# Performance work log

Hardware: AMD Instinct MI355X
Metric: run time of the kernel (lower is better)

The kernel has to match this reference:

```python
import jax, jax.numpy as jnp
import numpy as np

N_NODES = 50000
N_EDGES = 800000
D_NODE = 128
D_EDGE = 16
HID = 64
EPS = 1e-5


def _sage_conv(x, src, dst, Wl, bl, Wr, n_nodes):
    # PyG SAGEConv (mean aggr): out = lin_l(mean_{src->dst} x[src]) + lin_r(x)
    msg = x[src]                                        # [E, F] gather
    s = jax.ops.segment_sum(msg, dst, num_segments=n_nodes)   # [N, F]
    cnt = jax.ops.segment_sum(jnp.ones((src.shape[0],), x.dtype), dst,
                              num_segments=n_nodes)
    agg = s / jnp.maximum(cnt, 1.0)[:, None]
    return agg @ Wl.T + bl + x @ Wr.T


def _batchnorm(h, gamma, beta):
    # training-mode BN over node dim (biased variance, as in torch)
    mu = jnp.mean(h, axis=0)
    var = jnp.mean((h - mu) ** 2, axis=0)
    return gamma * (h - mu) / jnp.sqrt(var + EPS) + beta


def setup_inputs() -> dict:
    key = jax.random.key(0)
    ks = jax.random.split(key, 16)
    def lin(k, out_f, in_f):
        lim = 1.0 / np.sqrt(in_f)
        return jax.random.uniform(k, (out_f, in_f), jnp.float32, -lim, lim)
    x = jax.random.normal(ks[0], (N_NODES, D_NODE), jnp.float32)
    edge_index = jax.random.randint(ks[1], (2, N_EDGES), 0, N_NODES, jnp.int64)
    edge_attr = jax.random.normal(ks[2], (N_EDGES, D_EDGE), jnp.float32)
    return {
        "x": x, "edge_index": edge_index, "edge_attr": edge_attr,
        # SAGEConv 1
        "W1l": lin(ks[3], HID, D_NODE), "b1l": jnp.zeros((HID,), jnp.float32),
        "W1r": lin(ks[4], HID, D_NODE),
        "g1": jnp.ones((HID,), jnp.float32), "be1": jnp.zeros((HID,), jnp.float32),
        # SAGEConv 2
        "W2l": lin(ks[5], HID, HID), "b2l": jnp.zeros((HID,), jnp.float32),
        "W2r": lin(ks[6], HID, HID),
        "g2": jnp.ones((HID,), jnp.float32), "be2": jnp.zeros((HID,), jnp.float32),
        # edge MLP: (2*HID + D_EDGE) -> 128 -> 64 -> 2
        "Wm1": lin(ks[7], 128, 2 * HID + D_EDGE), "bm1": jnp.zeros((128,), jnp.float32),
        "Wm2": lin(ks[8], 64, 128), "bm2": jnp.zeros((64,), jnp.float32),
        "Wm3": lin(ks[9], 2, 64), "bm3": jnp.zeros((2,), jnp.float32),
    }


def reference(x, edge_index, edge_attr,
              W1l, b1l, W1r, g1, be1,
              W2l, b2l, W2r, g2, be2,
              Wm1, bm1, Wm2, bm2, Wm3, bm3):
    src, dst = edge_index[0], edge_index[1]
    n = x.shape[0]
    h = _sage_conv(x, src, dst, W1l, b1l, W1r, n)
    h = jax.nn.relu(_batchnorm(h, g1, be1))          # dropout = identity (eval)
    h = _sage_conv(h, src, dst, W2l, b2l, W2r, n)
    h = jax.nn.relu(_batchnorm(h, g2, be2))
    edge_in = jnp.concatenate([h[src], edge_attr, h[dst]], axis=1)  # [E, 144]
    z = jax.nn.relu(edge_in @ Wm1.T + bm1)
    z = jax.nn.relu(z @ Wm2.T + bm2)
    return z @ Wm3.T + bm3                           # [E, 2] logits
```

## Files before the change

kernel.cpp:

```cpp
#include <hip/hip_runtime.h>
#include <hip/hip_fp16.h>


#define EPS 1e-5f

typedef _Float16 h8 __attribute__((ext_vector_type(8)));
typedef float f32x4 __attribute__((ext_vector_type(4)));

__global__ __launch_bounds__(256) void k_prep_hist(
    const float* __restrict__ W1l, const float* __restrict__ W1r,
    const float* __restrict__ b1l,
    const float* __restrict__ W2l, const float* __restrict__ W2r,
    const float* __restrict__ b2l,
    const float* __restrict__ Wm1, const float* __restrict__ Wm2,
    float* __restrict__ Wt1, float* __restrict__ Wt2,
    float* __restrict__ bias1, float* __restrict__ bias2,
    __half* __restrict__ W2B, __half* __restrict__ W1B,
    const int* __restrict__ dst, int* __restrict__ deg, int E, int prepBlocks) {
  if ((int)blockIdx.x >= prepBlocks) {
    int e = (blockIdx.x - prepBlocks) * 256 + threadIdx.x;
    if (e < E) atomicAdd(&deg[dst[e]], 1);
    return;
  }
  int idx = blockIdx.x * 256 + threadIdx.x;
  if (idx < 16384) {
    int k = idx >> 7, f = idx & 127;
    Wt1[idx] = (f < 64) ? W1l[f * 128 + k] : W1r[(f - 64) * 128 + k];
    return;
  }
  idx -= 16384;
  if (idx < 8192) {
    int k = idx >> 7, f = idx & 127;
    Wt2[idx] = (f < 64) ? W2l[f * 64 + k] : W2r[(f - 64) * 64 + k];
    return;
  }
  idx -= 8192;
  if (idx < 128) { bias1[idx] = (idx < 64) ? 0.f : b1l[idx - 64]; return; }
  idx -= 128;
  if (idx < 128) { bias2[idx] = (idx < 64) ? 0.f : b2l[idx - 64]; return; }
  idx -= 128;
  if (idx < 8192) {
    int j = idx & 7, l = (idx >> 3) & 63, f = idx >> 9;
    int kc = f >> 2, tt = f & 3;
    int col = 16 * tt + (l & 15);
    int k = 32 * kc + (l >> 4) * 8 + j;
    W2B[idx] = __float2half(Wm2[col * 128 + k]);
    return;
  }
  idx -= 8192;
  if (idx < 20480) {
    int j = idx & 7, l = (idx >> 3) & 63, f = idx >> 9;
    int kc = f >> 3, nc = f & 7;
    int k = 32 * kc + (l >> 4) * 8 + j;
    int n = 16 * nc + (l & 15);
    float w;
    if (k < 64)       w = Wm1[n * 144 + k];
    else if (k < 128) w = Wm1[n * 144 + 80 + (k - 64)];
    else if (k < 144) w = Wm1[n * 144 + 64 + (k - 128)];
    else              w = 0.f;
    W1B[idx] = __float2half(w);
    return;
  }
}

__global__ __launch_bounds__(1024) void k_scan(
    const int* __restrict__ deg, int* __restrict__ rowptr,
    int* __restrict__ cursor, int N) {
  __shared__ int wsum[16];
  __shared__ int carry;
  const int lane = threadIdx.x & 63;
  const int w    = threadIdx.x >> 6;
  if (threadIdx.x == 0) carry = 0;
  __syncthreads();
  for (int base = 0; base < N; base += 1024) {
    int i = base + threadIdx.x;
    int v = (i < N) ? deg[i] : 0;
    int incl = v;
#pragma unroll
    for (int off = 1; off < 64; off <<= 1) {
      int t = __shfl_up(incl, off);
      if (lane >= off) incl += t;
    }
    if (lane == 63) wsum[w] = incl;
    __syncthreads();
    if (w == 0) {
      int ws_ = (lane < 16) ? wsum[lane] : 0;
      int wincl = ws_;
#pragma unroll
      for (int off = 1; off < 16; off <<= 1) {
        int t = __shfl_up(wincl, off);
        if (lane >= off) wincl += t;
      }
      if (lane < 16) wsum[lane] = wincl;
    }
    __syncthreads();
    int woff = carry + (w > 0 ? wsum[w - 1] : 0);
    int excl = woff + incl - v;
    if (i < N) { rowptr[i] = excl; cursor[i] = excl; }
    int tot = wsum[15];
    __syncthreads();
    if (threadIdx.x == 0) carry += tot;
    __syncthreads();
  }
  if (threadIdx.x == 0) rowptr[N] = carry;
}

__global__ __launch_bounds__(256) void k_fill(
    const int* __restrict__ src, const int* __restrict__ dst,
    const float* __restrict__ attr,
    int* __restrict__ cursor, int* __restrict__ csr_src,
    int* __restrict__ csr_dst, int* __restrict__ pos,
    __half* __restrict__ attrC, int E) {
  int e = blockIdx.x * 256 + threadIdx.x;
  if (e < E) {
    int d = dst[e];
    int p = atomicAdd(&cursor[d], 1);
    csr_src[p] = src[e];
    csr_dst[p] = d;
    pos[e] = p;
    const float4* at4 = (const float4*)attr;
    float4 a0 = at4[(size_t)e * 4 + 0];
    float4 a1 = at4[(size_t)e * 4 + 1];
    float4 a2 = at4[(size_t)e * 4 + 2];
    float4 a3 = at4[(size_t)e * 4 + 3];
    __half2 hh[8];
    hh[0] = __floats2half2_rn(a0.x, a0.y);
    hh[1] = __floats2half2_rn(a0.z, a0.w);
    hh[2] = __floats2half2_rn(a1.x, a1.y);
    hh[3] = __floats2half2_rn(a1.z, a1.w);
    hh[4] = __floats2half2_rn(a2.x, a2.y);
    hh[5] = __floats2half2_rn(a2.z, a2.w);
    hh[6] = __floats2half2_rn(a3.x, a3.y);
    hh[7] = __floats2half2_rn(a3.z, a3.w);
    *(uint4*)&attrC[(size_t)p * 16]     = *(uint4*)&hh[0];
    *(uint4*)&attrC[(size_t)p * 16 + 8] = *(uint4*)&hh[4];
  }
}

__global__ __launch_bounds__(256) void k_scatter_out(
    const float* __restrict__ out2, const int* __restrict__ pos,
    float* __restrict__ out, int E) {
  int e = blockIdx.x * 256 + threadIdx.x;
  if (e < E) {
    int p = pos[e];
    *(float2*)&out[(size_t)e * 2] = *(const float2*)&out2[(size_t)p * 2];
  }
}

template<int K, int MODE>
__global__ __launch_bounds__(256) void k_gemm(
    const float* __restrict__ X, const float* __restrict__ stats,
    const float* __restrict__ Wt, const float* __restrict__ bias,
    __half* __restrict__ outH, float* __restrict__ outF, int N, int Ftot) {
  __shared__ __align__(16) float Xs[32][68];
  __shared__ __align__(16) float Ws_[32][128];
  const int tid = threadIdx.x;
  const int tx  = tid & 15;
  const int ty  = tid >> 4;
  const int n0  = blockIdx.x * 64;
  float acc[4][8];
#pragma unroll
  for (int j = 0; j < 8; ++j) {
    float bv = bias[8 * tx + j];
#pragma unroll
    for (int i = 0; i < 4; ++i) acc[i][j] = bv;
  }
  for (int k0 = 0; k0 < K; k0 += 32) {
    __syncthreads();
#pragma unroll
    for (int l = 0; l < 2; ++l) {
      int idx = tid * 2 + l;
      int kq = idx & 7, n = idx >> 3;
      float4 xv = make_float4(0.f, 0.f, 0.f, 0.f);
      if (n0 + n < N) xv = *(const float4*)&X[(size_t)(n0 + n) * K + k0 + kq * 4];
      if (stats) {
        int kb = k0 + kq * 4;
        xv.x = fmaxf(xv.x * stats[128 + kb + 0] + stats[192 + kb + 0], 0.f);
        xv.y = fmaxf(xv.y * stats[128 + kb + 1] + stats[192 + kb + 1], 0.f);
        xv.z = fmaxf(xv.z * stats[128 + kb + 2] + stats[192 + kb + 2], 0.f);
        xv.w = fmaxf(xv.w * stats[128 + kb + 3] + stats[192 + kb + 3], 0.f);
      }
      Xs[kq * 4 + 0][n] = xv.x;
      Xs[kq * 4 + 1][n] = xv.y;
      Xs[kq * 4 + 2][n] = xv.z;
      Xs[kq * 4 + 3][n] = xv.w;
    }
#pragma unroll
    for (int l = 0; l < 4; ++l) {
      int idx = tid + l * 256;
      int kr = idx >> 5, fc = idx & 31;
      *(float4*)&Ws_[kr][fc * 4] =
          *(const float4*)&Wt[(size_t)(k0 + kr) * Ftot + fc * 4];
    }
    __syncthreads();
#pragma unroll
    for (int kk = 0; kk < 32; ++kk) {
      float4 a  = *(const float4*)&Xs[kk][4 * ty];
      float4 b0 = *(const float4*)&Ws_[kk][8 * tx];
      float4 b1 = *(const float4*)&Ws_[kk][8 * tx + 4];
      float aa[4] = {a.x, a.y, a.z, a.w};
      float bb[8] = {b0.x, b0.y, b0.z, b0.w, b1.x, b1.y, b1.z, b1.w};
#pragma unroll
      for (int i = 0; i < 4; ++i)
#pragma unroll
        for (int j = 0; j < 8; ++j) acc[i][j] += aa[i] * bb[j];
    }
  }
#pragma unroll
  for (int i = 0; i < 4; ++i) {
    int n = n0 + 4 * ty + i;
    if (n >= N) continue;
    if (tx < 8) {
      __half2 hh[4];
#pragma unroll
      for (int c = 0; c < 4; ++c)
        hh[c] = __floats2half2_rn(acc[i][2 * c], acc[i][2 * c + 1]);
      *(uint4*)&outH[(size_t)n * 64 + 8 * tx] = *(uint4*)hh;
    } else {
      float* cp = outF + (size_t)n * 64 + 8 * tx - 64;
      *(float4*)cp = make_float4(acc[i][0], acc[i][1], acc[i][2], acc[i][3]);
      *(float4*)(cp + 4) = make_float4(acc[i][4], acc[i][5], acc[i][6], acc[i][7]);
    }
  }
}

__global__ __launch_bounds__(256) void k_agg(
    const __half* __restrict__ qb, const float* __restrict__ pb,
    const int* __restrict__ rowptr, const int* __restrict__ csr_src,
    float* __restrict__ hpre, float* __restrict__ stats, int N) {
  __shared__ float red[512];
  const int tid  = threadIdx.x;
  const int w    = tid >> 6;
  const int lane = tid & 63;
  const int g    = lane >> 3, c = lane & 7;
  float lsum = 0.f, lsq = 0.f;
  const int wid = blockIdx.x * 4 + w;
  const int nw  = gridDim.x * 4;
  for (int n = wid; n < N; n += nw) {
    const int r0 = rowptr[n], r1 = rowptr[n + 1];
    float s[8] = {0.f, 0.f, 0.f, 0.f, 0.f, 0.f, 0.f, 0.f};
    for (int j = r0 + g; j < r1; j += 8) {
      int a = csr_src[j];
      uint4 rv = *(const uint4*)&qb[(size_t)a * 64 + 8 * c];
      const __half2* hp = (const __half2*)&rv;
#pragma unroll
      for (int q = 0; q < 4; ++q) {
        float2 f2 = __half22float2(hp[q]);
        s[2 * q]     += f2.x;
        s[2 * q + 1] += f2.y;
      }
    }
#pragma unroll
    for (int m = 8; m < 64; m <<= 1)
#pragma unroll
      for (int q = 0; q < 8; ++q) s[q] += __shfl_xor(s[q], m);
    float sv = s[0];
#pragma unroll
    for (int q = 1; q < 8; ++q) sv = (g == q) ? s[q] : sv;
    float cdeg = (float)(r1 - r0);
    cdeg = cdeg > 1.f ? cdeg : 1.f;
    const int f = 8 * c + g;
    float v = sv / cdeg + pb[(size_t)n * 64 + f];
    hpre[(size_t)n * 64 + f] = v;
    lsum += v;
    lsq  += v * v;
  }
  red[tid]       = lsum;
  red[256 + tid] = lsq;
  __syncthreads();
  if (tid < 64) {
    float ts = red[tid] + red[tid + 64] + red[tid + 128] + red[tid + 192];
    float tq = red[256 + tid] + red[256 + tid + 64] + red[256 + tid + 128] + red[256 + tid + 192];
    int f = 8 * (tid & 7) + (tid >> 3);
    atomicAdd(&stats[f], ts);
    atomicAdd(&stats[64 + f], tq);
  }
}

__global__ void k_finalize(float* stats, const float* __restrict__ g,
                           const float* __restrict__ be, int N) {
  int f = threadIdx.x;
  float inv_n = 1.0f / (float)N;
  float mean = stats[f] * inv_n;
  float var  = stats[64 + f] * inv_n - mean * mean;
  float s = g[f] * rsqrtf(var + EPS);
  stats[128 + f] = s;
  stats[192 + f] = be[f] - mean * s;
}

__global__ __launch_bounds__(256) void k_bn(
    const float* __restrict__ H1, const float* __restrict__ stats,
    __half* __restrict__ H2, int N) {
  int idx = blockIdx.x * 256 + threadIdx.x;
  if (idx >= N * 8) return;
  int n = idx >> 3, f8 = (idx & 7) * 8;
  float4 h0 = *(const float4*)&H1[(size_t)n * 64 + f8];
  float4 h1 = *(const float4*)&H1[(size_t)n * 64 + f8 + 4];
  const float* sc = stats + 128 + f8;
  const float* sh = stats + 192 + f8;
  __half2 hh[4];
  hh[0] = __floats2half2_rn(fmaxf(h0.x * sc[0] + sh[0], 0.f),
                            fmaxf(h0.y * sc[1] + sh[1], 0.f));
  hh[1] = __floats2half2_rn(fmaxf(h0.z * sc[2] + sh[2], 0.f),
                            fmaxf(h0.w * sc[3] + sh[3], 0.f));
  hh[2] = __floats2half2_rn(fmaxf(h1.x * sc[4] + sh[4], 0.f),
                            fmaxf(h1.y * sc[5] + sh[5], 0.f));
  hh[3] = __floats2half2_rn(fmaxf(h1.z * sc[6] + sh[6], 0.f),
                            fmaxf(h1.w * sc[7] + sh[7], 0.f));
  *(uint4*)&H2[(size_t)n * 64 + f8] = *(uint4*)hh;
}

__global__ __launch_bounds__(256, 2) void k_edge(
    const __half* __restrict__ H2, const __half* __restrict__ attrC,
    const int* __restrict__ csrc, const int* __restrict__ cdst,
    const __half* __restrict__ W1Bws, const __half* __restrict__ W2Bws,
    const float* __restrict__ bm1, const float* __restrict__ bm2,
    const float* __restrict__ Wm3, const float* __restrict__ bm3,
    float* __restrict__ out2, int E) {
  __shared__ __align__(16) _Float16 W1B[20480];
  __shared__ __align__(16) _Float16 W2B[8192];
  __shared__ __align__(16) _Float16 Z1f[64 * 136];

  const int tid  = threadIdx.x;
  const int lane = tid & 63;
  const int w    = tid >> 6;
  const int ln15 = lane & 15;
  const int quad = lane >> 4;

  for (int i = tid; i < 2560; i += 256)
    ((uint4*)W1B)[i] = ((const uint4*)W1Bws)[i];
  for (int i = tid; i < 1024; i += 256)
    ((uint4*)W2B)[i] = ((const uint4*)W2Bws)[i];

  float bm1v[8];
#pragma unroll
  for (int nc = 0; nc < 8; ++nc) bm1v[nc] = bm1[16 * nc + ln15];
  float bmv[4], w30[4], w31[4];
#pragma unroll
  for (int t = 0; t < 4; ++t) {
    bmv[t] = bm2[16 * t + ln15];
    w30[t] = Wm3[16 * t + ln15];
    w31[t] = Wm3[64 + 16 * t + ln15];
  }
  const float bm30 = bm3[0], bm31 = bm3[1];
  __syncthreads();

  const int nt = (E + 63) >> 6;
  const int rowoff = 16 * w + ln15;

  for (int t = blockIdx.x; t < nt; t += gridDim.x) {
    int er = (t << 6) + rowoff;
    if (er >= E) er = E - 1;
    const int s = csrc[er];
    const int d = cdst[er];

    h8 af0 = *(const h8*)&H2[(size_t)s * 64 + 8 * quad];
    h8 af1 = *(const h8*)&H2[(size_t)s * 64 + 32 + 8 * quad];
    h8 af2 = *(const h8*)&H2[(size_t)d * 64 + 8 * quad];
    h8 af3 = *(const h8*)&H2[(size_t)d * 64 + 32 + 8 * quad];
    h8 af4 = (h8){0, 0, 0, 0, 0, 0, 0, 0};
    if (quad < 2)
      af4 = *(const h8*)&attrC[(size_t)er * 16 + 8 * quad];

    f32x4 acc1[8];
#pragma unroll
    for (int nc = 0; nc < 8; ++nc)
      acc1[nc] = (f32x4){bm1v[nc], bm1v[nc], bm1v[nc], bm1v[nc]};
#pragma unroll
    for (int nc = 0; nc < 8; ++nc)
      acc1[nc] = __builtin_amdgcn_mfma_f32_16x16x32_f16(
          af0, *(const h8*)&W1B[((0 * 8 + nc) << 9) + (lane << 3)], acc1[nc], 0, 0, 0);
#pragma unroll
    for (int nc = 0; nc < 8; ++nc)
      acc1[nc] = __builtin_amdgcn_mfma_f32_16x16x32_f16(
          af1, *(const h8*)&W1B[((1 * 8 + nc) << 9) + (lane << 3)], acc1[nc], 0, 0, 0);
#pragma unroll
    for (int nc = 0; nc < 8; ++nc)
      acc1[nc] = __builtin_amdgcn_mfma_f32_16x16x32_f16(
          af2, *(const h8*)&W1B[((2 * 8 + nc) << 9) + (lane << 3)], acc1[nc], 0, 0, 0);
#pragma unroll
    for (int nc = 0; nc < 8; ++nc)
      acc1[nc] = __builtin_amdgcn_mfma_f32_16x16x32_f16(
          af3, *(const h8*)&W1B[((3 * 8 + nc) << 9) + (lane << 3)], acc1[nc], 0, 0, 0);
#pragma unroll
    for (int nc = 0; nc < 8; ++nc)
      acc1[nc] = __builtin_amdgcn_mfma_f32_16x16x32_f16(
          af4, *(const h8*)&W1B[((4 * 8 + nc) << 9) + (lane << 3)], acc1[nc], 0, 0, 0);

    const int ebase = 16 * w + 4 * quad;
#pragma unroll
    for (int nc = 0; nc < 8; ++nc)
#pragma unroll
      for (int r = 0; r < 4; ++r)
        Z1f[(ebase + r) * 136 + 16 * nc + ln15] =
            (_Float16)fmaxf(acc1[nc][r], 0.f);

    f32x4 acc2[4];
#pragma unroll
    for (int tt = 0; tt < 4; ++tt)
      acc2[tt] = (f32x4){bmv[tt], bmv[tt], bmv[tt], bmv[tt]};
#pragma unroll
    for (int kc = 0; kc < 4; ++kc) {
      h8 a = *(const h8*)&Z1f[(16 * w + ln15) * 136 + 32 * kc + 8 * quad];
#pragma unroll
      for (int tt = 0; tt < 4; ++tt) {
        h8 bf = *(const h8*)&W2B[((kc * 4 + tt) * 64 + lane) * 8];
        acc2[tt] = __builtin_amdgcn_mfma_f32_16x16x32_f16(a, bf, acc2[tt], 0, 0, 0);
      }
    }

    float p0[4], p1[4];
#pragma unroll
    for (int r = 0; r < 4; ++r) { p0[r] = 0.f; p1[r] = 0.f; }
#pragma unroll
    for (int tt = 0; tt < 4; ++tt)
#pragma unroll
      for (int r = 0; r < 4; ++r) {
        float z = fmaxf(acc2[tt][r], 0.f);
        p0[r] += z * w30[tt];
        p1[r] += z * w31[tt];
      }
#pragma unroll
    for (int r = 0; r < 4; ++r) {
#pragma unroll
      for (int m = 1; m < 16; m <<= 1) {
        p0[r] += __shfl_xor(p0[r], m);
        p1[r] += __shfl_xor(p1[r], m);
      }
      if (ln15 == 0) {
        int j = (t << 6) + 16 * w + 4 * quad + r;
        if (j < E)
          *(float2*)&out2[(size_t)j * 2] = make_float2(p0[r] + bm30, p1[r] + bm31);
      }
    }
  }
}

extern "C" void kernel_launch(void* const* d_in, const int* in_sizes, int n_in,
                              void* d_out, int out_size, void* d_ws, size_t ws_size,
                              hipStream_t stream) {
  const float* x    = (const float*)d_in[0];
  const int*   ei   = (const int*)d_in[1];
  const float* attr = (const float*)d_in[2];
  const float* W1l  = (const float*)d_in[3];
  const float* b1l  = (const float*)d_in[4];
  const float* W1r  = (const float*)d_in[5];
  const float* g1   = (const float*)d_in[6];
  const float* be1  = (const float*)d_in[7];
  const float* W2l  = (const float*)d_in[8];
  const float* b2l  = (const float*)d_in[9];
  const float* W2r  = (const float*)d_in[10];
  const float* g2   = (const float*)d_in[11];
  const float* be2  = (const float*)d_in[12];
  const float* Wm1  = (const float*)d_in[13];
  const float* bm1  = (const float*)d_in[14];
  const float* Wm2  = (const float*)d_in[15];
  const float* bm2  = (const float*)d_in[16];
  const float* Wm3  = (const float*)d_in[17];
  const float* bm3  = (const float*)d_in[18];
  float* out = (float*)d_out;

  const int N = in_sizes[0] / 128;
  const int E = in_sizes[1] / 2;
  const int* srcI = ei;
  const int* dstI = ei + E;

  float* ws = (float*)d_ws;
  const size_t NF = (size_t)N * 64;
  float*  P32 = ws;
  float*  H1  = ws + NF;
  __half* Q16 = (__half*)(ws + 2 * NF);
  float* small  = ws + 2 * NF + NF / 2;
  float* stats1 = small;
  float* stats2 = stats1 + 256;
  float* Wt1    = stats2 + 256;
  float* Wt2    = Wt1 + 16384;
  float* bias1  = Wt2 + 8192;
  float* bias2  = bias1 + 128;
  __half* W1B   = (__half*)(bias2 + 128);
  __half* W2B   = (__half*)(bias2 + 128 + 10240);
  int* rowptr = (int*)(bias2 + 128 + 10240 + 4096);
  int* cursor = rowptr + (N + 1);
  int* deg    = cursor + N;
  int* csrsrc = deg + N;
  int* csrdst = csrsrc + E;
  int* pos    = csrdst + E;
  __half* attrC = (__half*)(pos + E);

  __half* H2  = Q16;
  float* out2 = H1;

  hipMemsetAsync(deg, 0, (size_t)N * sizeof(int), stream);
  hipMemsetAsync(stats1, 0, 512 * sizeof(float), stream);

  const int eBlocks = (E + 255) / 256;
  const int prepBlocks = (53504 + 255) / 256;
  k_prep_hist<<<prepBlocks + eBlocks, 256, 0, stream>>>(
      W1l, W1r, b1l, W2l, W2r, b2l, Wm1, Wm2,
      Wt1, Wt2, bias1, bias2, W2B, W1B,
      dstI, deg, E, prepBlocks);
  k_scan<<<1, 1024, 0, stream>>>(deg, rowptr, cursor, N);
  k_fill<<<eBlocks, 256, 0, stream>>>(srcI, dstI, attr, cursor,
                                      csrsrc, csrdst, pos, attrC, E);

  const int mTiles = (N + 63) / 64;

  k_gemm<128, 0><<<mTiles, 256, 0, stream>>>(x, nullptr, Wt1, bias1, Q16, P32, N, 128);
  k_agg<<<1024, 256, 0, stream>>>(Q16, P32, rowptr, csrsrc, H1, stats1, N);
  k_finalize<<<1, 64, 0, stream>>>(stats1, g1, be1, N);

  k_gemm<64, 0><<<mTiles, 256, 0, stream>>>(H1, stats1, Wt2, bias2, Q16, P32, N, 128);
  k_agg<<<1024, 256, 0, stream>>>(Q16, P32, rowptr, csrsrc, H1, stats2, N);
  k_finalize<<<1, 64, 0, stream>>>(stats2, g2, be2, N);

  k_bn<<<(N * 8 + 255) / 256, 256, 0, stream>>>(H1, stats2, H2, N);

  k_edge<<<1024, 256, 0, stream>>>(H2, attrC, csrsrc, csrdst,
                                   W1B, W2B, bm1, bm2, Wm3, bm3, out2, E);
  k_scatter_out<<<eBlocks, 256, 0, stream>>>(out2, pos, out, E);
}
```

Measured before the change: 567.9 us.

## Software-pipeline edge MLP gathers with next-tile prefetch and reordered MFMA chains

The edge MLP loop now prefetches the H2 row gathers and edge attributes for the next tile, and the src/dst indices two tiles ahead, into registers while the current tile's MFMAs run. The goal is to hide the latency of the dependent irregular global loads. The first-layer MFMA loop is also reordered to finish one output chunk at a time, which reduces live accumulator registers to offset the extra prefetch registers. The trade-offs are higher register pressure, which may lower occupancy, and a long dependent MFMA chain per chunk.

```diff
diff --git a/kernel.cpp b/kernel.cpp
--- a/kernel.cpp
+++ b/kernel.cpp
@@ -346,54 +346,66 @@
   __syncthreads();
 
   const int nt = (E + 63) >> 6;
+  const int G  = gridDim.x;
   const int rowoff = 16 * w + ln15;
-
-  for (int t = blockIdx.x; t < nt; t += gridDim.x) {
-    int er = (t << 6) + rowoff;
+  const int t0 = blockIdx.x;
+
+  int sN, dN;
+  h8 af0, af1, af2, af3, af4;
+  {
+    int er = (t0 << 6) + rowoff;
     if (er >= E) er = E - 1;
-    const int s = csrc[er];
-    const int d = cdst[er];
-
-    h8 af0 = *(const h8*)&H2[(size_t)s * 64 + 8 * quad];
-    h8 af1 = *(const h8*)&H2[(size_t)s * 64 + 32 + 8 * quad];
-    h8 af2 = *(const h8*)&H2[(size_t)d * 64 + 8 * quad];
-    h8 af3 = *(const h8*)&H2[(size_t)d * 64 + 32 + 8 * quad];
-    h8 af4 = (h8){0, 0, 0, 0, 0, 0, 0, 0};
-    if (quad < 2)
-      af4 = *(const h8*)&attrC[(size_t)er * 16 + 8 * quad];
-
-    f32x4 acc1[8];
-#pragma unroll
-    for (int nc = 0; nc < 8; ++nc)
-      acc1[nc] = (f32x4){bm1v[nc], bm1v[nc], bm1v[nc], bm1v[nc]};
-#pragma unroll
-    for (int nc = 0; nc < 8; ++nc)
-      acc1[nc] = __builtin_amdgcn_mfma_f32_16x16x32_f16(
-          af0, *(const h8*)&W1B[((0 * 8 + nc) << 9) + (lane << 3)], acc1[nc], 0, 0, 0);
-#pragma unroll
-    for (int nc = 0; nc < 8; ++nc)
-      acc1[nc] = __builtin_amdgcn_mfma_f32_16x16x32_f16(
-          af1, *(const h8*)&W1B[((1 * 8 + nc) << 9) + (lane << 3)], acc1[nc], 0, 0, 0);
-#pragma unroll
-    for (int nc = 0; nc < 8; ++nc)
-      acc1[nc] = __builtin_amdgcn_mfma_f32_16x16x32_f16(
-          af2, *(const h8*)&W1B[((2 * 8 + nc) << 9) + (lane << 3)], acc1[nc], 0, 0, 0);
-#pragma unroll
-    for (int nc = 0; nc < 8; ++nc)
-      acc1[nc] = __builtin_amdgcn_mfma_f32_16x16x32_f16(
-          af3, *(const h8*)&W1B[((3 * 8 + nc) << 9) + (lane << 3)], acc1[nc], 0, 0, 0);
-#pragma unroll
-    for (int nc = 0; nc < 8; ++nc)
-      acc1[nc] = __builtin_amdgcn_mfma_f32_16x16x32_f16(
-          af4, *(const h8*)&W1B[((4 * 8 + nc) << 9) + (lane << 3)], acc1[nc], 0, 0, 0);
+    int s = csrc[er], d = cdst[er];
+    af0 = *(const h8*)&H2[(size_t)s * 64 + 8 * quad];
+    af1 = *(const h8*)&H2[(size_t)s * 64 + 32 + 8 * quad];
+    af2 = *(const h8*)&H2[(size_t)d * 64 + 8 * quad];
+    af3 = *(const h8*)&H2[(size_t)d * 64 + 32 + 8 * quad];
+    af4 = (h8){0, 0, 0, 0, 0, 0, 0, 0};
+    if (quad < 2) af4 = *(const h8*)&attrC[(size_t)er * 16 + 8 * quad];
+  }
+  {
+    int er = ((t0 + G) << 6) + rowoff;
+    if (er >= E) er = E - 1;
+    sN = csrc[er]; dN = cdst[er];
+  }
+
+  for (int t = t0; t < nt; t += G) {
+    h8 nf0 = *(const h8*)&H2[(size_t)sN * 64 + 8 * quad];
+    h8 nf1 = *(const h8*)&H2[(size_t)sN * 64 + 32 + 8 * quad];
+    h8 nf2 = *(const h8*)&H2[(size_t)dN * 64 + 8 * quad];
+    h8 nf3 = *(const h8*)&H2[(size_t)dN * 64 + 32 + 8 * quad];
+    h8 nf4 = (h8){0, 0, 0, 0, 0, 0, 0, 0};
+    {
+      int erN = ((t + G) << 6) + rowoff;
+      if (erN >= E) erN = E - 1;
+      if (quad < 2) nf4 = *(const h8*)&attrC[(size_t)erN * 16 + 8 * quad];
+    }
+    int sNN, dNN;
+    {
+      int er2 = ((t + 2 * G) << 6) + rowoff;
+      if (er2 >= E) er2 = E - 1;
+      sNN = csrc[er2]; dNN = cdst[er2];
+    }
 
     const int ebase = 16 * w + 4 * quad;
 #pragma unroll
-    for (int nc = 0; nc < 8; ++nc)
-#pragma unroll
-      for (int r = 0; r < 4; ++r)
-        Z1f[(ebase + r) * 136 + 16 * nc + ln15] =
-            (_Float16)fmaxf(acc1[nc][r], 0.f);
+    for (int nc = 0; nc < 8; ++nc) {
+      f32x4 a1 = (f32x4){bm1v[nc], bm1v[nc], bm1v[nc], bm1v[nc]};
+      a1 = __builtin_amdgcn_mfma_f32_16x16x32_f16(
+          af0, *(const h8*)&W1B[((0 * 8 + nc) << 9) + (lane << 3)], a1, 0, 0, 0);
+      a1 = __builtin_amdgcn_mfma_f32_16x16x32_f16(
+          af1, *(const h8*)&W1B[((1 * 8 + nc) << 9) + (lane << 3)], a1, 0, 0, 0);
+      a1 = __builtin_amdgcn_mfma_f32_16x16x32_f16(
+          af2, *(const h8*)&W1B[((2 * 8 + nc) << 9) + (lane << 3)], a1, 0, 0, 0);
+      a1 = __builtin_amdgcn_mfma_f32_16x16x32_f16(
+          af3, *(const h8*)&W1B[((3 * 8 + nc) << 9) + (lane << 3)], a1, 0, 0, 0);
+      a1 = __builtin_amdgcn_mfma_f32_16x16x32_f16(
+          af4, *(const h8*)&W1B[((4 * 8 + nc) << 9) + (lane << 3)], a1, 0, 0, 0);
+      Z1f[(ebase + 0) * 136 + 16 * nc + ln15] = (_Float16)fmaxf(a1[0], 0.f);
+      Z1f[(ebase + 1) * 136 + 16 * nc + ln15] = (_Float16)fmaxf(a1[1], 0.f);
+      Z1f[(ebase + 2) * 136 + 16 * nc + ln15] = (_Float16)fmaxf(a1[2], 0.f);
+      Z1f[(ebase + 3) * 136 + 16 * nc + ln15] = (_Float16)fmaxf(a1[3], 0.f);
+    }
 
     f32x4 acc2[4];
 #pragma unroll
@@ -433,6 +445,9 @@
           *(float2*)&out2[(size_t)j * 2] = make_float2(p0[r] + bm30, p1[r] + bm31);
       }
     }
+
+    af0 = nf0; af1 = nf1; af2 = nf2; af3 = nf3; af4 = nf4;
+    sN = sNN; dN = dNN;
   }
 }
 
```

After: 583.0 us. 2.7% more time.
